# Optimization experiments

Measured on AMD Instinct MI355X. Metric: run time of the kernel, lower is better.

The kernel has to match this reference:

```python
import jax, jax.numpy as jnp
import numpy as np

N = 30000
E = 480000
VDIM = 512
HID = 32
EPS_BN = 1e-5
EPS_COS = 1e-8


def setup_inputs() -> dict:
    key = jax.random.key(0)
    ks = jax.random.split(key, 12)
    inp = {}
    inp["x"] = jax.random.normal(ks[0], (N, 2), dtype=jnp.float32)
    inp["visual"] = jax.random.normal(ks[1], (N, VDIM), dtype=jnp.float32)
    inp["edge_index"] = jax.random.randint(ks[2], (2, E), 0, N, dtype=jnp.int64)
    # input_mlp: Linear(2,32) -> BN(32) -> PReLU -> Dropout(0) -> Linear(32,32)
    inp["w1"] = jax.random.normal(ks[3], (HID, 2), dtype=jnp.float32) * 0.1
    inp["b1"] = jnp.zeros((HID,), dtype=jnp.float32)
    inp["gamma"] = jnp.ones((HID,), dtype=jnp.float32)
    inp["beta"] = jnp.zeros((HID,), dtype=jnp.float32)
    inp["prelu_a"] = jnp.asarray(0.25, dtype=jnp.float32)  # torch default: single shared slope
    inp["w2"] = jax.random.normal(ks[4], (HID, HID), dtype=jnp.float32) * 0.1
    inp["b2"] = jnp.zeros((HID,), dtype=jnp.float32)
    # CMCosConv(32, 32, 512): linear over cos-weighted mean aggregation
    inp["wc"] = jax.random.normal(ks[5], (HID, HID), dtype=jnp.float32) * 0.1
    inp["bc"] = jnp.zeros((HID,), dtype=jnp.float32)
    # gcn_projection_face: Linear(32,1)
    inp["wp"] = jax.random.normal(ks[6], (1, HID), dtype=jnp.float32) * 0.1
    inp["bp"] = jnp.zeros((1,), dtype=jnp.float32)
    return inp


def reference(x, visual, edge_index, w1, b1, gamma, beta, prelu_a, w2, b2, wc, bc, wp, bp):
    # ---- input_mlp ----
    h = x @ w1.T + b1  # [N,32]
    mu = jnp.mean(h, axis=0)
    var = jnp.mean((h - mu) ** 2, axis=0)  # biased, training-mode BN
    h = (h - mu) * jax.lax.rsqrt(var + EPS_BN) * gamma + beta
    h = jnp.where(h >= 0, h, prelu_a * h)  # PReLU, single slope
    h = h @ w2.T + b2  # [N,32]

    # ---- CMCosConv: edge weight = cos(visual_src, visual_dst); cos-weighted mean agg; linear ----
    vn = visual / jnp.maximum(jnp.linalg.norm(visual, axis=-1, keepdims=True), EPS_COS)  # [N,512]
    src = edge_index[0]
    dst = edge_index[1]
    w = jnp.sum(vn[src] * vn[dst], axis=-1)  # [E] cosine per edge (memory-bound gathers)
    msg = w[:, None] * h[src]  # [E,32]
    agg = jax.ops.segment_sum(msg, dst, num_segments=N)  # [N,32]
    deg = jax.ops.segment_sum(jnp.ones_like(w), dst, num_segments=N)  # [N]
    agg = agg / jnp.maximum(deg, 1.0)[:, None]  # mean aggregation
    hc = agg @ wc.T + bc  # [N,32]; conv_activation=None -> identity

    # ---- projection ----
    scores = (hc @ wp.T + bp).squeeze(-1)  # [N]
    return scores
```

## Files before the change

kernel.cpp:

```cpp
#include <hip/hip_runtime.h>
#include <hip/hip_fp16.h>
#include <math.h>

#define N_NODES 30000
#define E_EDGES 480000
#define VD      512
#define HID     32
#define BUCKET  3750
#define K1_BLOCKS 512
#define BIG_ENC 1048576.0

#define SARR_OFF 60000
#define PART_OFF 90000
#define INV_OFF  92560
#define NV_BYTE_OFF   524288u
#define EI16_BYTE_OFF 15884288u

__device__ inline void atomAddF64(double* p, double v) {
#if defined(__HIP_PLATFORM_AMD__)
    unsafeAtomicAdd(p, v);
#else
    atomicAdd(p, v);
#endif
}

__device__ inline int edot4(unsigned int a, unsigned int b, int c) {
#if __has_builtin(__builtin_amdgcn_sdot4)
    return __builtin_amdgcn_sdot4((int)a, (int)b, (int)c, false);
#else
    int r = c;
    r += (int)(signed char)(a)       * (int)(signed char)(b);
    r += (int)(signed char)(a >> 8)  * (int)(signed char)(b >> 8);
    r += (int)(signed char)(a >> 16) * (int)(signed char)(b >> 16);
    r += (int)(signed char)(a >> 24) * (int)(signed char)(b >> 24);
    return r;
#endif
}

__device__ inline unsigned int pack4i8(float x0, float x1, float x2, float x3, float sc) {
    int q0 = (int)rintf(x0 * sc);
    int q1 = (int)rintf(x1 * sc);
    int q2 = (int)rintf(x2 * sc);
    int q3 = (int)rintf(x3 * sc);
    return (unsigned int)(q0 & 255) | ((unsigned int)(q1 & 255) << 8) |
           ((unsigned int)(q2 & 255) << 16) | ((unsigned int)(q3 & 255) << 24);
}

__global__ void __launch_bounds__(256) k1_prep(
        const float* __restrict__ x,
        const float* __restrict__ visual,
        const int* __restrict__ ei,
        float* __restrict__ ws, int i8mode) {
    const int t      = threadIdx.x;
    const int gid    = blockIdx.x * blockDim.x + t;
    const int stride = gridDim.x * blockDim.x;
    const int lane   = t & 63;

    for (int i = gid; i < 2 * N_NODES; i += stride) ws[i] = 0.f;

    {
        unsigned int* ei16 = (unsigned int*)((char*)ws + EI16_BYTE_OFF);
        for (int e = gid; e < E_EDGES; e += stride) {
            unsigned int s = (unsigned int)ei[e];
            unsigned int d = (unsigned int)ei[E_EDGES + e];
            ei16[e] = s | (d << 16);
        }
    }

    {
        __shared__ float red[4][5];
        float s0 = 0.f, s1 = 0.f, s00 = 0.f, s11 = 0.f, s01 = 0.f;
        for (int i = gid; i < N_NODES; i += stride) {
            float2 v = ((const float2*)x)[i];
            s0  += v.x;       s1  += v.y;
            s00 += v.x * v.x; s11 += v.y * v.y;
            s01 += v.x * v.y;
        }
        for (int o = 32; o; o >>= 1) {
            s0  += __shfl_xor(s0,  o, 64);
            s1  += __shfl_xor(s1,  o, 64);
            s00 += __shfl_xor(s00, o, 64);
            s11 += __shfl_xor(s11, o, 64);
            s01 += __shfl_xor(s01, o, 64);
        }
        int wv = t >> 6;
        if (lane == 0) {
            red[wv][0] = s0; red[wv][1] = s1; red[wv][2] = s00;
            red[wv][3] = s11; red[wv][4] = s01;
        }
        __syncthreads();
        if (t < 5) {
            ws[PART_OFF + blockIdx.x * 5 + t] =
                red[0][t] + red[1][t] + red[2][t] + red[3][t];
        }
    }

    char*  nvis8 = (char*)ws + NV_BYTE_OFF;
    float* inv   = ws + INV_OFF;
    const int grp  = (lane >> 4);
    const int sub  = lane & 15;
    const int wave  = gid >> 6;
    const int nwave = stride >> 6;
    for (int base = wave * 4; base < N_NODES; base += nwave * 4) {
        const int node = base + grp;
        const float4* row = (const float4*)(visual + (size_t)node * VD);
        float4 v0 = row[sub];
        float4 v1 = row[sub + 16];
        float4 v2 = row[sub + 32];
        float4 v3 = row[sub + 48];
        float4 v4 = row[sub + 64];
        float4 v5 = row[sub + 80];
        float4 v6 = row[sub + 96];
        float4 v7 = row[sub + 112];
        float p = 0.f, am = 0.f;
        #define ACCUM(vv) \
            p += vv.x*vv.x + vv.y*vv.y + vv.z*vv.z + vv.w*vv.w; \
            am = fmaxf(am, fmaxf(fmaxf(fabsf(vv.x), fabsf(vv.y)), \
                                 fmaxf(fabsf(vv.z), fabsf(vv.w))));
        ACCUM(v0) ACCUM(v1) ACCUM(v2) ACCUM(v3)
        ACCUM(v4) ACCUM(v5) ACCUM(v6) ACCUM(v7)
        #undef ACCUM
        for (int o = 8; o; o >>= 1) {
            p  += __shfl_xor(p, o, 64);
            am  = fmaxf(am, __shfl_xor(am, o, 64));
        }
        float r = 1.0f / fmaxf(sqrtf(p), 1e-8f);
        if (i8mode) {
            float vnmax = am * r;
            float qsc   = 127.0f / fmaxf(vnmax, 1e-20f);
            float rs    = r * qsc;
            unsigned int* orow = (unsigned int*)(nvis8 + (size_t)node * 512);
            orow[sub]       = pack4i8(v0.x, v0.y, v0.z, v0.w, rs);
            orow[sub + 16]  = pack4i8(v1.x, v1.y, v1.z, v1.w, rs);
            orow[sub + 32]  = pack4i8(v2.x, v2.y, v2.z, v2.w, rs);
            orow[sub + 48]  = pack4i8(v3.x, v3.y, v3.z, v3.w, rs);
            orow[sub + 64]  = pack4i8(v4.x, v4.y, v4.z, v4.w, rs);
            orow[sub + 80]  = pack4i8(v5.x, v5.y, v5.z, v5.w, rs);
            orow[sub + 96]  = pack4i8(v6.x, v6.y, v6.z, v6.w, rs);
            orow[sub + 112] = pack4i8(v7.x, v7.y, v7.z, v7.w, rs);
            if (sub == 0) inv[node] = vnmax * (1.0f / 127.0f);
        } else if (sub == 0) {
            inv[node] = r;
        }
    }
}

__global__ void __launch_bounds__(256) k2_sarr(
        const float* __restrict__ x,
        const float* __restrict__ w1, const float* __restrict__ b1,
        const float* __restrict__ gamma, const float* __restrict__ beta,
        const float* __restrict__ prelu_a,
        const float* __restrict__ w2, const float* __restrict__ b2,
        const float* __restrict__ wc, const float* __restrict__ wp,
        const float* __restrict__ ws_ro,
        float* __restrict__ sarr, int i8mode) {
    __shared__ float red[4][5];
    __shared__ float s_S[5];
    __shared__ float s_scale[HID], s_shift[HID], s_u[HID], s_w1a[HID], s_w1b[HID];
    __shared__ float s_wpc[HID];
    __shared__ float s_sb;
    const float* part = ws_ro + PART_OFF;
    const float* qs   = ws_ro + INV_OFF;
    const int t    = threadIdx.x;
    const int lane = t & 63;

    {
        float S[5] = {0.f, 0.f, 0.f, 0.f, 0.f};
        for (int j = t; j < K1_BLOCKS; j += 256) {
            #pragma unroll
            for (int c = 0; c < 5; ++c) S[c] += part[j * 5 + c];
        }
        #pragma unroll
        for (int c = 0; c < 5; ++c)
            for (int o = 32; o; o >>= 1) S[c] += __shfl_xor(S[c], o, 64);
        int wv = t >> 6;
        if (lane == 0) {
            #pragma unroll
            for (int c = 0; c < 5; ++c) red[wv][c] = S[c];
        }
        __syncthreads();
        if (t < 5) s_S[t] = red[0][t] + red[1][t] + red[2][t] + red[3][t];
        __syncthreads();
    }

    if (t < HID) {
        float wpck = 0.f;
        for (int j = 0; j < HID; ++j) wpck += wp[j] * wc[j * HID + t];
        s_wpc[t] = wpck;
        const float invN = 1.0f / (float)N_NODES;
        float m0  = s_S[0] * invN, m1 = s_S[1] * invN;
        float v0  = fmaxf(s_S[2] * invN - m0 * m0, 0.f);
        float v1  = fmaxf(s_S[3] * invN - m1 * m1, 0.f);
        float c01 = s_S[4] * invN - m0 * m1;
        float a0 = w1[2 * t], a1 = w1[2 * t + 1];
        float mean = a0 * m0 + a1 * m1 + b1[t];
        float var  = fmaxf(a0 * a0 * v0 + a1 * a1 * v1 + 2.f * a0 * a1 * c01, 0.f);
        float rs    = 1.0f / sqrtf(var + 1e-5f);
        float scale = gamma[t] * rs;
        s_scale[t] = scale;
        s_shift[t] = beta[t] - mean * scale;
        s_w1a[t] = a0; s_w1b[t] = a1;
    }
    __syncthreads();
    if (t < HID) {
        float uu = 0.f;
        for (int k = 0; k < HID; ++k) uu += s_wpc[k] * w2[k * HID + t];
        s_u[t] = uu;
    }
    if (t == 0) {
        float sb = 0.f;
        for (int k = 0; k < HID; ++k) sb += s_wpc[k] * b2[k];
        s_sb = sb;
    }
    __syncthreads();
    const float aslope = prelu_a[0];
    const float sb = s_sb;
    for (int i = blockIdx.x * blockDim.x + t; i < N_NODES; i += gridDim.x * blockDim.x) {
        float2 xv = ((const float2*)x)[i];
        float sacc = sb;
        #pragma unroll
        for (int c = 0; c < HID; ++c) {
            float h  = s_w1a[c] * xv.x + s_w1b[c] * xv.y + b1[c];
            float tt = h * s_scale[c] + s_shift[c];
            tt = tt >= 0.f ? tt : aslope * tt;
            sacc += tt * s_u[c];
        }
        sarr[i] = i8mode ? sacc * qs[i] : sacc;
    }
}

__global__ void __launch_bounds__(256) k3_edge8(const unsigned int* __restrict__ ei16,
                                                const float* __restrict__ ws_ro,
                                                double* __restrict__ accD,
                                                const float* __restrict__ sq) {
    const char* nvb = (const char*)ws_ro + NV_BYTE_OFF;
    const int lane = threadIdx.x & 63;
    const int sub  = lane & 7;
    const int g    = lane >> 3;
    const int r    = blockIdx.x & 7;
    const int q    = (blockIdx.x >> 3) * (blockDim.x >> 6) + (threadIdx.x >> 6);
    const int nq   = (gridDim.x >> 3) * (blockDim.x >> 6);
    const int nchunk = E_EDGES >> 6;

    for (int c = q; c < nchunk; c += nq) {
        int idx = (c << 6) + lane;
        unsigned int sd = ei16[idx];
        int s = (int)(sd & 0xffffu);
        int d = (int)(sd >> 16);
        bool mine = (s / BUCKET == r);
        float mys = mine ? sq[s] : 0.f;
        unsigned long long m = __ballot(mine);
        while (m) {
            int j0 = __ffsll(m) - 1;  m &= m - 1;
            int cnt = 1;
            int j1 = j0, j2 = j0, j3 = j0, j4 = j0, j5 = j0, j6 = j0, j7 = j0;
            if (m) { j1 = __ffsll(m) - 1; m &= m - 1; cnt = 2; }
            if (m) { j2 = __ffsll(m) - 1; m &= m - 1; cnt = 3; }
            if (m) { j3 = __ffsll(m) - 1; m &= m - 1; cnt = 4; }
            if (m) { j4 = __ffsll(m) - 1; m &= m - 1; cnt = 5; }
            if (m) { j5 = __ffsll(m) - 1; m &= m - 1; cnt = 6; }
            if (m) { j6 = __ffsll(m) - 1; m &= m - 1; cnt = 7; }
            if (m) { j7 = __ffsll(m) - 1; m &= m - 1; cnt = 8; }

            int jsel = (g < 4) ? ((g < 2) ? (g == 0 ? j0 : j1) : (g == 2 ? j2 : j3))
                               : ((g < 6) ? (g == 4 ? j4 : j5) : (g == 6 ? j6 : j7));
            int   se = __shfl(s,   jsel, 64);
            int   de = __shfl(d,   jsel, 64);
            float sv = __shfl(mys, jsel, 64);

            const uint4* sa = (const uint4*)(nvb + ((size_t)se << 9)) + sub;
            const uint4* da = (const uint4*)(nvb + ((size_t)de << 9)) + sub;
            uint4 A0 = sa[0];
            uint4 B0 = da[0];
            uint4 A1 = sa[8];
            uint4 B1 = da[8];
            uint4 A2 = sa[16];
            uint4 B2 = da[16];
            uint4 A3 = sa[24];
            uint4 B3 = da[24];

            int p = 0;
            p = edot4(A0.x, B0.x, p);
            p = edot4(A0.y, B0.y, p);
            p = edot4(A0.z, B0.z, p);
            p = edot4(A0.w, B0.w, p);
            p = edot4(A1.x, B1.x, p);
            p = edot4(A1.y, B1.y, p);
            p = edot4(A1.z, B1.z, p);
            p = edot4(A1.w, B1.w, p);
            p = edot4(A2.x, B2.x, p);
            p = edot4(A2.y, B2.y, p);
            p = edot4(A2.z, B2.z, p);
            p = edot4(A2.w, B2.w, p);
            p = edot4(A3.x, B3.x, p);
            p = edot4(A3.y, B3.y, p);
            p = edot4(A3.z, B3.z, p);
            p = edot4(A3.w, B3.w, p);

            p += __shfl_xor(p, 4, 64);
            p += __shfl_xor(p, 2, 64);
            p += __shfl_xor(p, 1, 64);

            if (sub == 0 && g < cnt) {
                atomAddF64(&accD[de], (double)((float)p * sv) + BIG_ENC);
            }
        }
    }
}

__global__ void __launch_bounds__(256) k3_edge32(const int* __restrict__ ei,
                                                 const float* __restrict__ visual,
                                                 const float* __restrict__ inv,
                                                 const float* __restrict__ sarr,
                                                 double* __restrict__ accD) {
    int wave  = (blockIdx.x * blockDim.x + threadIdx.x) >> 6;
    int lane  = threadIdx.x & 63;
    int nwave = (gridDim.x * blockDim.x) >> 6;
    for (int e = wave; e < E_EDGES; e += nwave) {
        int s = ei[e];
        int d = ei[E_EDGES + e];
        const float4* ra = (const float4*)(visual + (size_t)s * VD);
        const float4* rb = (const float4*)(visual + (size_t)d * VD);
        float4 a0 = ra[lane];
        float4 b0 = rb[lane];
        float4 a1 = ra[lane + 64];
        float4 b1 = rb[lane + 64];
        float p = a0.x*b0.x + a0.y*b0.y + a0.z*b0.z + a0.w*b0.w
                + a1.x*b1.x + a1.y*b1.y + a1.z*b1.z + a1.w*b1.w;
        for (int o = 32; o; o >>= 1) p += __shfl_xor(p, o, 64);
        if (lane == 0) {
            float w = p * inv[s] * inv[d];
            atomAddF64(&accD[d], (double)(w * sarr[s]) + BIG_ENC);
        }
    }
}

__global__ void k4_final(const double* __restrict__ accD,
                         const float* __restrict__ qs,
                         const float* __restrict__ bc, const float* __restrict__ wp,
                         const float* __restrict__ bp, float* __restrict__ out,
                         int n, int i8mode) {
    float K = bp[0];
    #pragma unroll
    for (int j = 0; j < HID; ++j) K += wp[j] * bc[j];
    for (int i = blockIdx.x * blockDim.x + threadIdx.x; i < n; i += gridDim.x * blockDim.x) {
        double total = accD[i];
        int cnt = (int)__double2ll_rn(total * (1.0 / BIG_ENC));
        float a = (float)(total - (double)cnt * BIG_ENC);
        if (i8mode) a *= qs[i];
        out[i] = a / (float)max(cnt, 1) + K;
    }
}

extern "C" void kernel_launch(void* const* d_in, const int* in_sizes, int n_in,
                              void* d_out, int out_size, void* d_ws, size_t ws_size,
                              hipStream_t stream) {
    const float* x       = (const float*)d_in[0];
    const float* visual  = (const float*)d_in[1];
    const int*   ei      = (const int*)  d_in[2];
    const float* w1      = (const float*)d_in[3];
    const float* b1      = (const float*)d_in[4];
    const float* gamma   = (const float*)d_in[5];
    const float* beta    = (const float*)d_in[6];
    const float* prelu_a = (const float*)d_in[7];
    const float* w2      = (const float*)d_in[8];
    const float* b2      = (const float*)d_in[9];
    const float* wc      = (const float*)d_in[10];
    const float* bc      = (const float*)d_in[11];
    const float* wp      = (const float*)d_in[12];
    const float* bp      = (const float*)d_in[13];
    float* out = (float*)d_out;

    float*  ws   = (float*)d_ws;
    double* accD = (double*)d_ws;
    float*  sarr = ws + SARR_OFF;
    float*  inv  = ws + INV_OFF;
    unsigned int* ei16 = (unsigned int*)((char*)d_ws + EI16_BYTE_OFF);

    bool i8ok = ws_size >= (size_t)EI16_BYTE_OFF + (size_t)E_EDGES * 4;

    k1_prep<<<K1_BLOCKS, 256, 0, stream>>>(x, visual, ei, ws, i8ok ? 1 : 0);
    k2_sarr<<<512, 256, 0, stream>>>(x, w1, b1, gamma, beta, prelu_a, w2, b2, wc, wp,
                                     ws, sarr, i8ok ? 1 : 0);
    if (i8ok) {
        k3_edge8<<<4096, 256, 0, stream>>>(ei16, ws, accD, sarr);
    } else {
        k3_edge32<<<4096, 256, 0, stream>>>(ei, visual, inv, sarr, accD);
    }
    k4_final<<<120, 256, 0, stream>>>(accD, inv, bc, wp, bp, out, N_NODES, i8ok ? 1 : 0);
}
```

Before: 167.8 us.

## Bin edges by source/destination bucket with counting sort for dense edge processing

Replaces the per-chunk ballot filtering in the edge kernel with a two-pass counting sort. The prep kernel builds per-block histograms over an 8x8 grid of source and destination buckets, and the second kernel scans them and scatters the packed edges into bucket-sorted order. The edge kernel then walks a contiguous range per source bucket with no wasted lanes, and the destination bucket ordering improves gather locality. In exchange it adds histogram and scatter work plus extra workspace, and the scatter writes are irregular.

```diff
diff --git a/kernel.cpp b/kernel.cpp
--- a/kernel.cpp
+++ b/kernel.cpp
@@ -8,13 +8,18 @@
 #define HID     32
 #define BUCKET  3750
 #define K1_BLOCKS 512
+#define NBS     500
+#define EPB     960
 #define BIG_ENC 1048576.0
 
 #define SARR_OFF 60000
 #define PART_OFF 90000
 #define INV_OFF  92560
-#define NV_BYTE_OFF   524288u
-#define EI16_BYTE_OFF 15884288u
+#define BINSTART_BYTE_OFF 490240u
+#define NV_BYTE_OFF       524288u
+#define EI16_BYTE_OFF     15884288u
+#define HIST_BYTE_OFF     17804288u
+#define WS_NEED           17935360u
 
 __device__ inline void atomAddF64(double* p, double v) {
 #if defined(__HIP_PLATFORM_AMD__)
@@ -52,19 +57,26 @@
         const int* __restrict__ ei,
         float* __restrict__ ws, int i8mode) {
     const int t      = threadIdx.x;
-    const int gid    = blockIdx.x * blockDim.x + t;
+    const int b      = blockIdx.x;
+    const int gid    = b * blockDim.x + t;
     const int stride = gridDim.x * blockDim.x;
     const int lane   = t & 63;
 
     for (int i = gid; i < 2 * N_NODES; i += stride) ws[i] = 0.f;
 
-    {
-        unsigned int* ei16 = (unsigned int*)((char*)ws + EI16_BYTE_OFF);
-        for (int e = gid; e < E_EDGES; e += stride) {
+    if (i8mode && b < NBS) {
+        __shared__ unsigned int lh[64];
+        unsigned int* hist = (unsigned int*)((char*)ws + HIST_BYTE_OFF);
+        if (t < 64) lh[t] = 0u;
+        __syncthreads();
+        for (int j = t; j < EPB; j += 256) {
+            int e = b * EPB + j;
             unsigned int s = (unsigned int)ei[e];
             unsigned int d = (unsigned int)ei[E_EDGES + e];
-            ei16[e] = s | (d << 16);
-        }
+            atomicAdd(&lh[(s / BUCKET) * 8 + (d / BUCKET)], 1u);
+        }
+        __syncthreads();
+        if (t < 64) hist[t * 512 + b] = lh[t];
     }
 
     {
@@ -90,7 +102,7 @@
         }
         __syncthreads();
         if (t < 5) {
-            ws[PART_OFF + blockIdx.x * 5 + t] =
+            ws[PART_OFF + b * 5 + t] =
                 red[0][t] + red[1][t] + red[2][t] + red[3][t];
         }
     }
@@ -147,21 +159,24 @@
 
 __global__ void __launch_bounds__(256) k2_sarr(
         const float* __restrict__ x,
+        const int* __restrict__ ei,
         const float* __restrict__ w1, const float* __restrict__ b1,
         const float* __restrict__ gamma, const float* __restrict__ beta,
         const float* __restrict__ prelu_a,
         const float* __restrict__ w2, const float* __restrict__ b2,
         const float* __restrict__ wc, const float* __restrict__ wp,
-        const float* __restrict__ ws_ro,
+        float* __restrict__ ws,
         float* __restrict__ sarr, int i8mode) {
     __shared__ float red[4][5];
     __shared__ float s_S[5];
     __shared__ float s_scale[HID], s_shift[HID], s_u[HID], s_w1a[HID], s_w1b[HID];
     __shared__ float s_wpc[HID];
     __shared__ float s_sb;
-    const float* part = ws_ro + PART_OFF;
-    const float* qs   = ws_ro + INV_OFF;
+    __shared__ unsigned int s_tot[64], s_my[64], s_cur[64];
+    const float* part = ws + PART_OFF;
+    const float* qs   = ws + INV_OFF;
     const int t    = threadIdx.x;
+    const int b    = blockIdx.x;
     const int lane = t & 63;
 
     {
@@ -215,7 +230,7 @@
     __syncthreads();
     const float aslope = prelu_a[0];
     const float sb = s_sb;
-    for (int i = blockIdx.x * blockDim.x + t; i < N_NODES; i += gridDim.x * blockDim.x) {
+    for (int i = b * blockDim.x + t; i < N_NODES; i += gridDim.x * blockDim.x) {
         float2 xv = ((const float2*)x)[i];
         float sacc = sb;
         #pragma unroll
@@ -227,12 +242,55 @@
         }
         sarr[i] = i8mode ? sacc * qs[i] : sacc;
     }
-}
-
-__global__ void __launch_bounds__(256) k3_edge8(const unsigned int* __restrict__ ei16,
-                                                const float* __restrict__ ws_ro,
-                                                double* __restrict__ accD,
-                                                const float* __restrict__ sq) {
+
+    if (i8mode && b < NBS) {
+        const unsigned int* hist = (const unsigned int*)((const char*)ws + HIST_BYTE_OFF);
+        unsigned int* binstart   = (unsigned int*)((char*)ws + BINSTART_BYTE_OFF);
+        unsigned int* ei16s      = (unsigned int*)((char*)ws + EI16_BYTE_OFF);
+
+        const int k   = t >> 2;
+        const int prt = t & 3;
+        unsigned int tot = 0, my = 0;
+        const unsigned int* H = hist + k * 512;
+        for (int i = prt * 125; i < (prt + 1) * 125; ++i) {
+            unsigned int v = H[i];
+            tot += v;
+            if (i < b) my += v;
+        }
+        tot += __shfl_down(tot, 2, 4); tot += __shfl_down(tot, 1, 4);
+        my  += __shfl_down(my,  2, 4); my  += __shfl_down(my,  1, 4);
+        if (prt == 0) { s_tot[k] = tot; s_my[k] = my; }
+        __syncthreads();
+        if (t < 64) {
+            unsigned int v = s_tot[t];
+            for (int o = 1; o < 64; o <<= 1) {
+                unsigned int u = __shfl_up(v, o, 64);
+                if (t >= o) v += u;
+            }
+            unsigned int excl = v - s_tot[t];
+            s_cur[t] = excl + s_my[t];
+            if (b == 0) {
+                binstart[t] = excl;
+                if (t == 63) binstart[64] = v;
+            }
+        }
+        __syncthreads();
+        for (int j = t; j < EPB; j += 256) {
+            int e = b * EPB + j;
+            unsigned int s = (unsigned int)ei[e];
+            unsigned int d = (unsigned int)ei[E_EDGES + e];
+            int bin = (int)(s / BUCKET) * 8 + (int)(d / BUCKET);
+            unsigned int slot = atomicAdd(&s_cur[bin], 1u);
+            ei16s[slot] = s | (d << 16);
+        }
+    }
+}
+
+__global__ void __launch_bounds__(256) k3_dense8(const unsigned int* __restrict__ ei16s,
+                                                 const unsigned int* __restrict__ binstart,
+                                                 const float* __restrict__ ws_ro,
+                                                 double* __restrict__ accD,
+                                                 const float* __restrict__ sq) {
     const char* nvb = (const char*)ws_ro + NV_BYTE_OFF;
     const int lane = threadIdx.x & 63;
     const int sub  = lane & 7;
@@ -240,70 +298,55 @@
     const int r    = blockIdx.x & 7;
     const int q    = (blockIdx.x >> 3) * (blockDim.x >> 6) + (threadIdx.x >> 6);
     const int nq   = (gridDim.x >> 3) * (blockDim.x >> 6);
-    const int nchunk = E_EDGES >> 6;
-
-    for (int c = q; c < nchunk; c += nq) {
-        int idx = (c << 6) + lane;
-        unsigned int sd = ei16[idx];
-        int s = (int)(sd & 0xffffu);
-        int d = (int)(sd >> 16);
-        bool mine = (s / BUCKET == r);
-        float mys = mine ? sq[s] : 0.f;
-        unsigned long long m = __ballot(mine);
-        while (m) {
-            int j0 = __ffsll(m) - 1;  m &= m - 1;
-            int cnt = 1;
-            int j1 = j0, j2 = j0, j3 = j0, j4 = j0, j5 = j0, j6 = j0, j7 = j0;
-            if (m) { j1 = __ffsll(m) - 1; m &= m - 1; cnt = 2; }
-            if (m) { j2 = __ffsll(m) - 1; m &= m - 1; cnt = 3; }
-            if (m) { j3 = __ffsll(m) - 1; m &= m - 1; cnt = 4; }
-            if (m) { j4 = __ffsll(m) - 1; m &= m - 1; cnt = 5; }
-            if (m) { j5 = __ffsll(m) - 1; m &= m - 1; cnt = 6; }
-            if (m) { j6 = __ffsll(m) - 1; m &= m - 1; cnt = 7; }
-            if (m) { j7 = __ffsll(m) - 1; m &= m - 1; cnt = 8; }
-
-            int jsel = (g < 4) ? ((g < 2) ? (g == 0 ? j0 : j1) : (g == 2 ? j2 : j3))
-                               : ((g < 6) ? (g == 4 ? j4 : j5) : (g == 6 ? j6 : j7));
-            int   se = __shfl(s,   jsel, 64);
-            int   de = __shfl(d,   jsel, 64);
-            float sv = __shfl(mys, jsel, 64);
-
-            const uint4* sa = (const uint4*)(nvb + ((size_t)se << 9)) + sub;
-            const uint4* da = (const uint4*)(nvb + ((size_t)de << 9)) + sub;
-            uint4 A0 = sa[0];
-            uint4 B0 = da[0];
-            uint4 A1 = sa[8];
-            uint4 B1 = da[8];
-            uint4 A2 = sa[16];
-            uint4 B2 = da[16];
-            uint4 A3 = sa[24];
-            uint4 B3 = da[24];
-
-            int p = 0;
-            p = edot4(A0.x, B0.x, p);
-            p = edot4(A0.y, B0.y, p);
-            p = edot4(A0.z, B0.z, p);
-            p = edot4(A0.w, B0.w, p);
-            p = edot4(A1.x, B1.x, p);
-            p = edot4(A1.y, B1.y, p);
-            p = edot4(A1.z, B1.z, p);
-            p = edot4(A1.w, B1.w, p);
-            p = edot4(A2.x, B2.x, p);
-            p = edot4(A2.y, B2.y, p);
-            p = edot4(A2.z, B2.z, p);
-            p = edot4(A2.w, B2.w, p);
-            p = edot4(A3.x, B3.x, p);
-            p = edot4(A3.y, B3.y, p);
-            p = edot4(A3.z, B3.z, p);
-            p = edot4(A3.w, B3.w, p);
-
-            p += __shfl_xor(p, 4, 64);
-            p += __shfl_xor(p, 2, 64);
-            p += __shfl_xor(p, 1, 64);
-
-            if (sub == 0 && g < cnt) {
-                atomAddF64(&accD[de], (double)((float)p * sv) + BIG_ENC);
-            }
+    const int rs   = (int)binstart[r * 8];
+    const int re   = (int)binstart[r * 8 + 8];
+
+    for (int e8 = rs + q * 8; e8 < re; e8 += nq * 8) {
+        int li = e8 + (lane & 7);
+        if (li >= re) li = re - 1;
+        unsigned int sd = ei16s[li];
+        unsigned int sdg = __shfl(sd, g, 8);
+        int se = (int)(sdg & 0xffffu);
+        int de = (int)(sdg >> 16);
+        bool valid = (e8 + g) < re;
+        float sv = 0.f;
+        if (sub == 0 && valid) sv = sq[se];
+
+        const uint4* sa = (const uint4*)(nvb + ((size_t)se << 9)) + sub;
+        const uint4* da = (const uint4*)(nvb + ((size_t)de << 9)) + sub;
+        uint4 A0 = sa[0];
+        uint4 B0 = da[0];
+        uint4 A1 = sa[8];
+        uint4 B1 = da[8];
+        uint4 A2 = sa[16];
+        uint4 B2 = da[16];
+        uint4 A3 = sa[24];
+        uint4 B3 = da[24];
+
+        int p = 0;
+        p = edot4(A0.x, B0.x, p);
+        p = edot4(A0.y, B0.y, p);
+        p = edot4(A0.z, B0.z, p);
+        p = edot4(A0.w, B0.w, p);
+        p = edot4(A1.x, B1.x, p);
+        p = edot4(A1.y, B1.y, p);
+        p = edot4(A1.z, B1.z, p);
+        p = edot4(A1.w, B1.w, p);
+        p = edot4(A2.x, B2.x, p);
+        p = edot4(A2.y, B2.y, p);
+        p = edot4(A2.z, B2.z, p);
+        p = edot4(A2.w, B2.w, p);
+        p = edot4(A3.x, B3.x, p);
+        p = edot4(A3.y, B3.y, p);
+        p = edot4(A3.z, B3.z, p);
+        p = edot4(A3.w, B3.w, p);
+
+        p += __shfl_xor(p, 4, 64);
+        p += __shfl_xor(p, 2, 64);
+        p += __shfl_xor(p, 1, 64);
+
+        if (sub == 0 && valid) {
+            atomAddF64(&accD[de], (double)((float)p * sv) + BIG_ENC);
         }
     }
 }
@@ -375,15 +418,16 @@
     double* accD = (double*)d_ws;
     float*  sarr = ws + SARR_OFF;
     float*  inv  = ws + INV_OFF;
-    unsigned int* ei16 = (unsigned int*)((char*)d_ws + EI16_BYTE_OFF);
-
-    bool i8ok = ws_size >= (size_t)EI16_BYTE_OFF + (size_t)E_EDGES * 4;
+    unsigned int* ei16s    = (unsigned int*)((char*)d_ws + EI16_BYTE_OFF);
+    unsigned int* binstart = (unsigned int*)((char*)d_ws + BINSTART_BYTE_OFF);
+
+    bool i8ok = ws_size >= (size_t)WS_NEED;
 
     k1_prep<<<K1_BLOCKS, 256, 0, stream>>>(x, visual, ei, ws, i8ok ? 1 : 0);
-    k2_sarr<<<512, 256, 0, stream>>>(x, w1, b1, gamma, beta, prelu_a, w2, b2, wc, wp,
+    k2_sarr<<<512, 256, 0, stream>>>(x, ei, w1, b1, gamma, beta, prelu_a, w2, b2, wc, wp,
                                      ws, sarr, i8ok ? 1 : 0);
     if (i8ok) {
-        k3_edge8<<<4096, 256, 0, stream>>>(ei16, ws, accD, sarr);
+        k3_dense8<<<4096, 256, 0, stream>>>(ei16s, binstart, ws, accD, sarr);
     } else {
         k3_edge32<<<4096, 256, 0, stream>>>(ei, visual, inv, sarr, accD);
     }
```

New measurement: 177.6 us. 1.06x slower.
